# Performance work log

Hardware: AMD Instinct MI355X
Metric: run time of the kernel (lower is better)

Reference implementation:

```python
import jax, jax.numpy as jnp
import numpy as np

B, H, W, C = 8, 128, 128, 256
NH = 8
HD = C // NH
WS = 8           # window size
SS = 4           # shift size
N = WS * WS      # tokens per window
SCALE = HD ** -0.5
EPS = 1e-5


def _rel_pos_index():
    coords = np.stack(np.meshgrid(np.arange(WS), np.arange(WS), indexing='ij'))  # [2,WS,WS]
    cf = coords.reshape(2, -1)                                                   # [2,N]
    rel = (cf[:, :, None] - cf[:, None, :]).transpose(1, 2, 0)                   # [N,N,2]
    rel[..., 0] += WS - 1
    rel[..., 1] += WS - 1
    rel[..., 0] *= 2 * WS - 1
    return rel.sum(-1)  # [N,N] indices into (2*WS-1)^2 table

RPI = jnp.asarray(_rel_pos_index())


def _attn_mask():
    img = np.zeros((H, W))
    slices = (slice(0, -WS), slice(-WS, -SS), slice(-SS, None))
    cnt = 0
    for hs in slices:
        for ws_ in slices:
            img[hs, ws_] = cnt
            cnt += 1
    mw = img.reshape(H // WS, WS, W // WS, WS).transpose(0, 2, 1, 3).reshape(-1, N)  # [nW,N]
    am = mw[:, None, :] - mw[:, :, None]
    return jnp.asarray(np.where(am != 0, -100.0, 0.0).astype(np.float32))  # [nW,N,N]

ATTN_MASK = _attn_mask()


def _ln(x, g, b):
    m = jnp.mean(x, -1, keepdims=True)
    v = jnp.var(x, -1, keepdims=True)
    return (x - m) * jax.lax.rsqrt(v + EPS) * g + b


def setup_inputs() -> dict:
    key = jax.random.key(0)
    ks = jax.random.split(key, 8)
    s = 0.02
    return {
        'x': jax.random.normal(ks[0], (B, H * W, C), jnp.float32),
        'qkv_w': jax.random.normal(ks[1], (C, 3 * C), jnp.float32) * s,
        'qkv_b': jnp.zeros((3 * C,), jnp.float32),
        'proj_w': jax.random.normal(ks[2], (C, C), jnp.float32) * s,
        'proj_b': jnp.zeros((C,), jnp.float32),
        'rpb': jax.random.normal(ks[3], ((2 * WS - 1) ** 2, NH), jnp.float32) * s,
        'g1': jnp.ones((C,), jnp.float32), 'b1': jnp.zeros((C,), jnp.float32),
        'g2': jnp.ones((C,), jnp.float32), 'b2': jnp.zeros((C,), jnp.float32),
        'fc1_w': jax.random.normal(ks[4], (C, 4 * C), jnp.float32) * s,
        'fc1_b': jnp.zeros((4 * C,), jnp.float32),
        'fc2_w': jax.random.normal(ks[5], (4 * C, C), jnp.float32) * s,
        'fc2_b': jnp.zeros((C,), jnp.float32),
    }


def reference(x, qkv_w, qkv_b, proj_w, proj_b, rpb, g1, b1, g2, b2,
              fc1_w, fc1_b, fc2_w, fc2_b):
    nW = (H // WS) * (W // WS)
    shortcut = x
    h = _ln(x, g1, b1).reshape(B, H, W, C)
    # cyclic shift
    h = jnp.roll(h, (-SS, -SS), axis=(1, 2))
    # window partition -> (B*nW, N, C)
    win = h.reshape(B, H // WS, WS, W // WS, WS, C).transpose(0, 1, 3, 2, 4, 5).reshape(-1, N, C)
    qkv = (win @ qkv_w + qkv_b).reshape(-1, N, 3, NH, HD).transpose(2, 0, 3, 1, 4)  # [3,B_,NH,N,HD]
    q, k, v = qkv[0] * SCALE, qkv[1], qkv[2]
    attn = jnp.einsum('bhnd,bhmd->bhnm', q, k)                    # [B_,NH,N,N]
    bias = rpb[RPI].transpose(2, 0, 1)                             # [NH,N,N]
    attn = attn + bias[None]
    attn = attn.reshape(B, nW, NH, N, N) + ATTN_MASK[None, :, None]
    attn = jax.nn.softmax(attn.reshape(-1, NH, N, N), axis=-1)
    out = jnp.einsum('bhnm,bhmd->bhnd', attn, v).transpose(0, 2, 1, 3).reshape(-1, N, C)
    out = out @ proj_w + proj_b
    # window reverse + reverse shift
    out = out.reshape(B, H // WS, W // WS, WS, WS, C).transpose(0, 1, 3, 2, 4, 5).reshape(B, H, W, C)
    out = jnp.roll(out, (SS, SS), axis=(1, 2)).reshape(B, H * W, C)
    x = shortcut + out
    hm = _ln(x, g2, b2)
    hm = jax.nn.gelu(hm @ fc1_w + fc1_b, approximate=False) @ fc2_w + fc2_b
    return x + hm
```

## Files before the change

### kernel.cpp

```cpp
#include <hip/hip_runtime.h>
#include <math.h>


#define NWIN_TOTAL 2048
#define TOK_TOTAL  131072
#define SCALE_Q    0.17677669529663687f
#define LOG2E      1.4426950408889634f

typedef unsigned short u16;
typedef __attribute__((ext_vector_type(4))) unsigned short u16x4;
typedef __attribute__((ext_vector_type(8))) unsigned short u16x8;
typedef __attribute__((ext_vector_type(8))) short bf16x8;
typedef __attribute__((ext_vector_type(4))) float f32x4;

#define AS1 __attribute__((address_space(1)))
#define AS3 __attribute__((address_space(3)))
#define GLOAD_LDS16(g, l) \
  __builtin_amdgcn_global_load_lds((const AS1 unsigned int*)(g), (AS3 unsigned int*)(l), 16, 0, 0)

__device__ __forceinline__ float bf2f(u16 u) {
  union { unsigned int i; float f; } c; c.i = ((unsigned int)u) << 16; return c.f;
}
__device__ __forceinline__ u16 f2bf(float f) {
  union { float f; unsigned int i; } c; c.f = f;
  return (u16)((c.i + 0x7fff + ((c.i >> 16) & 1)) >> 16);
}
__device__ __forceinline__ int regid3(int h) { return h < 120 ? 0 : (h < 124 ? 1 : 2); }
__device__ __forceinline__ float gelu_f(float v) {
  float t = exp2f(v * fmaf(v * v, 0.10294423f, 2.3022082f));
  return v * t * __builtin_amdgcn_rcpf(t + 1.0f);
}

__device__ __forceinline__ int win_tok_to_t(int g, int n) {
  int b = g >> 8, wi = g & 255;
  int wr = wi >> 4, wc = wi & 15;
  int hs = wr * 8 + (n >> 3), ws2 = wc * 8 + (n & 7);
  int h = (hs + 4) & 127, w = (ws2 + 4) & 127;
  return (b << 14) + (h << 7) + w;
}

__global__ __launch_bounds__(256)
void wconv_kernel(const float* __restrict__ w, u16* __restrict__ wt, int K, int N)
{
  int i = blockIdx.x * 256 + threadIdx.x;
  if (i >= K * N) return;
  int k = i / N, n = i - k * N;
  wt[(size_t)n * K + k] = f2bf(w[i]);
}

__global__ __launch_bounds__(1024)
void qln_kernel(const float* __restrict__ x, const float* __restrict__ g1,
                const float* __restrict__ b1, const u16* __restrict__ qkvT,
                const float* __restrict__ qkv_b,
                u16* __restrict__ qb, u16* __restrict__ kb, u16* __restrict__ vb,
                int g0)
{
  __shared__ u16 Aln[16384];
  const int tid = threadIdx.x, wid = tid >> 6, lane = tid & 63;
  const int l15 = lane & 15, g = lane >> 4;
  const int bwi = blockIdx.x;
  const int gw = g0 + bwi;

  {
    const int row = tid >> 4;
    const int cq = (tid & 15) * 16;
    const int t = win_tok_to_t(gw, row);
    const float* src = x + (size_t)t * 256 + cq;
    float vals[16];
    float s = 0.f, q = 0.f;
#pragma unroll
    for (int i = 0; i < 4; ++i) {
      float4 v = ((const float4*)src)[i];
      vals[i*4] = v.x; vals[i*4+1] = v.y; vals[i*4+2] = v.z; vals[i*4+3] = v.w;
      s += v.x + v.y + v.z + v.w;
      q += v.x*v.x + v.y*v.y + v.z*v.z + v.w*v.w;
    }
    s += __shfl_xor(s, 1, 64); q += __shfl_xor(q, 1, 64);
    s += __shfl_xor(s, 2, 64); q += __shfl_xor(q, 2, 64);
    s += __shfl_xor(s, 4, 64); q += __shfl_xor(q, 4, 64);
    s += __shfl_xor(s, 8, 64); q += __shfl_xor(q, 8, 64);
    float mean = s * 0.00390625f;
    float rstd = rsqrtf(q * 0.00390625f - mean * mean + 1e-5f);
#pragma unroll
    for (int i = 0; i < 2; ++i) {
      const int col = cq + i * 8;
      u16x8 o;
#pragma unroll
      for (int j = 0; j < 8; ++j)
        o[j] = f2bf((vals[i*8+j] - mean) * rstd * g1[col+j] + b1[col+j]);
      const int gran = col >> 3;
      *(u16x8*)((char*)Aln + row * 512 + ((gran ^ (row & 7)) << 4)) = o;
    }
  }
  __syncthreads();

  f32x4 acc[4][3];
#pragma unroll
  for (int m = 0; m < 4; ++m)
#pragma unroll
    for (int n = 0; n < 3; ++n) acc[m][n] = (f32x4){0.f, 0.f, 0.f, 0.f};
  const int colb = wid * 48;
#pragma unroll
  for (int ks = 0; ks < 8; ++ks) {
    bf16x8 af[4], bw[3];
#pragma unroll
    for (int m = 0; m < 4; ++m) {
      const int tok = m * 16 + l15;
      const int gran = ks * 4 + g;
      af[m] = *(const bf16x8*)&Aln[tok * 256 + ((gran ^ (tok & 7)) << 3)];
    }
#pragma unroll
    for (int n = 0; n < 3; ++n)
      bw[n] = *(const bf16x8*)(qkvT + (size_t)(colb + n * 16 + l15) * 256 + ks * 32 + g * 8);
#pragma unroll
    for (int m = 0; m < 4; ++m)
#pragma unroll
      for (int n = 0; n < 3; ++n)
        acc[m][n] = __builtin_amdgcn_mfma_f32_16x16x32_bf16(af[m], bw[n], acc[m][n], 0, 0, 0);
  }

#pragma unroll
  for (int n = 0; n < 3; ++n) {
    const int col16 = colb + n * 16;
    const float bv = qkv_b[col16 + l15];
    const int s = col16 >> 8, head = (col16 >> 5) & 7, hd = col16 & 31;
    if (s == 2) {
      const size_t obase = ((size_t)bwi << 14) + ((size_t)head << 11) + (size_t)(hd + l15) * 64;
#pragma unroll
      for (int m = 0; m < 4; ++m) {
        const int tok0 = m * 16 + g * 4;
        u16x4 pk;
#pragma unroll
        for (int r = 0; r < 4; ++r) pk[r] = f2bf(acc[m][n][r] + bv);
        *(u16x4*)&vb[obase + tok0] = pk;
      }
    } else {
      u16* qdst = (s == 0) ? qb : kb;
      const float scl = (s == 0) ? SCALE_Q * LOG2E : 1.f;
      const size_t obase = ((size_t)bwi << 14) + ((size_t)head << 11) + hd + l15;
#pragma unroll
      for (int m = 0; m < 4; ++m)
#pragma unroll
        for (int r = 0; r < 4; ++r) {
          const int tok = m * 16 + g * 4 + r;
          qdst[obase + ((size_t)tok << 5)] = f2bf((acc[m][n][r] + bv) * scl);
        }
    }
  }
}

__global__ __launch_bounds__(512)
void awp_kernel(const u16* __restrict__ qb, const u16* __restrict__ kb,
                const u16* __restrict__ vt, const float* __restrict__ rpb,
                const u16* __restrict__ pjT, const float* __restrict__ pjb,
                const float* __restrict__ x, float* __restrict__ out, int g0)
{
  __shared__ union {
    u16 pl[8][2048];
    u16 aoL[16384];
    float rep[8192];
  } sb;
  __shared__ float rl[1800];
  const int tid = threadIdx.x, hh = tid >> 6, lane = tid & 63;
  const int l15 = lane & 15, g = lane >> 4;
  const int bw = blockIdx.x;

  for (int i = tid; i < 1800; i += 512) {
    unsigned int h2 = (unsigned)i / 225u;
    unsigned int rem = (unsigned)i - h2 * 225u;
    unsigned int aa = rem / 15u, bb = rem - aa * 15u;
    rl[i] = rpb[(aa * 15u + 14u - bb) * 8u + h2] * LOG2E;
  }
  __syncthreads();

  const size_t base = ((size_t)(bw * 8 + hh)) << 11;

  bf16x8 qf[4], kf[4];
#pragma unroll
  for (int f = 0; f < 4; ++f) {
    qf[f] = *(const bf16x8*)(qb + base + (size_t)(f * 16 + l15) * 32 + g * 8);
    kf[f] = *(const bf16x8*)(kb + base + (size_t)(f * 16 + l15) * 32 + g * 8);
  }
  f32x4 acc[4][4];
#pragma unroll
  for (int mf = 0; mf < 4; ++mf)
#pragma unroll
    for (int nf = 0; nf < 4; ++nf) acc[mf][nf] = (f32x4){0.f, 0.f, 0.f, 0.f};
#pragma unroll
  for (int mf = 0; mf < 4; ++mf)
#pragma unroll
    for (int nf = 0; nf < 4; ++nf)
      acc[mf][nf] = __builtin_amdgcn_mfma_f32_16x16x32_bf16(kf[mf], qf[nf], acc[mf][nf], 0, 0, 0);

  const int gwin = g0 + bw;
  const int wrw = (gwin >> 4) & 15, wcw = gwin & 15;
  const bool edge = (wrw == 15) || (wcw == 15);
  const int i2b = g >> 1;
  const int j2b = (g & 1) * 4;
#pragma unroll
  for (int nf = 0; nf < 4; ++nf) {
    const int n = nf * 16 + l15;
    const int i1 = n >> 3, j1 = n & 7;
    const int rid1 = edge ? regid3(wrw * 8 + i1) * 3 + regid3(wcw * 8 + j1) : 0;
#pragma unroll
    for (int mf = 0; mf < 4; ++mf) {
      const int i2 = mf * 2 + i2b;
      const int ib = hh * 225 + (i1 - i2 + 7) * 15 + (j2b - j1 + 7);
      const int r2a = edge ? regid3(wrw * 8 + i2) * 3 : 0;
#pragma unroll
      for (int r = 0; r < 4; ++r) {
        float b = rl[ib + r];
        if (edge) {
          int rid2 = r2a + regid3(wcw * 8 + j2b + r);
          if (rid2 != rid1) b -= 144.2695f;
        }
        acc[mf][nf][r] += b;
      }
    }
  }

  float inv[4];
#pragma unroll
  for (int nf = 0; nf < 4; ++nf) {
    float m0 = -1e30f;
#pragma unroll
    for (int mf = 0; mf < 4; ++mf)
#pragma unroll
      for (int r = 0; r < 4; ++r) m0 = fmaxf(m0, acc[mf][nf][r]);
    m0 = fmaxf(m0, __shfl_xor(m0, 16, 64));
    m0 = fmaxf(m0, __shfl_xor(m0, 32, 64));
    float s = 0.f;
#pragma unroll
    for (int mf = 0; mf < 4; ++mf)
#pragma unroll
      for (int r = 0; r < 4; ++r) {
        float p = exp2f(acc[mf][nf][r] - m0);
        acc[mf][nf][r] = p;
        s += p;
      }
    s += __shfl_xor(s, 16, 64);
    s += __shfl_xor(s, 32, 64);
    inv[nf] = 1.f / s;
  }

  bf16x8 vf[2][2];
#pragma unroll
  for (int df = 0; df < 2; ++df)
#pragma unroll
    for (int ks = 0; ks < 2; ++ks)
      vf[df][ks] = *(const bf16x8*)(vt + base + (size_t)(df * 16 + l15) * 64 + ks * 32 + g * 8);
  f32x4 accO[4][2];
#pragma unroll
  for (int nf = 0; nf < 4; ++nf)
#pragma unroll
    for (int df = 0; df < 2; ++df) accO[nf][df] = (f32x4){0.f, 0.f, 0.f, 0.f};
  char* plw = (char*)sb.pl[hh];
#pragma unroll
  for (int ks = 0; ks < 2; ++ks) {
#pragma unroll
    for (int nf = 0; nf < 4; ++nf) {
      const int n = nf * 16 + l15;
      const int swz = (n & 3) << 4;
#pragma unroll
      for (int mm = 0; mm < 2; ++mm) {
        const int mf = ks * 2 + mm;
        float p0 = acc[mf][nf][0] * inv[nf], p1 = acc[mf][nf][1] * inv[nf];
        float p2 = acc[mf][nf][2] * inv[nf], p3 = acc[mf][nf][3] * inv[nf];
        unsigned int pa, pb;
        asm("v_cvt_pk_bf16_f32 %0, %1, %2" : "=v"(pa) : "v"(p0), "v"(p1));
        asm("v_cvt_pk_bf16_f32 %0, %1, %2" : "=v"(pb) : "v"(p2), "v"(p3));
        uint2 w; w.x = pa; w.y = pb;
        *(uint2*)(plw + ((n * 64 + mm * 32 + g * 8) ^ swz)) = w;
      }
    }
#pragma unroll
    for (int nf = 0; nf < 4; ++nf) {
      const int n = nf * 16 + l15;
      const int swz = (n & 3) << 4;
      bf16x8 pf = *(const bf16x8*)(plw + ((n * 64 + g * 16) ^ swz));
#pragma unroll
      for (int df = 0; df < 2; ++df)
        accO[nf][df] = __builtin_amdgcn_mfma_f32_16x16x32_bf16(pf, vf[df][ks], accO[nf][df], 0, 0, 0);
    }
  }

  __syncthreads();
#pragma unroll
  for (int nf = 0; nf < 4; ++nf)
#pragma unroll
    for (int r = 0; r < 4; ++r) {
      const int tok = nf * 16 + g * 4 + r;
#pragma unroll
      for (int df = 0; df < 2; ++df) {
        const int ch = hh * 32 + df * 16 + l15;
        *(u16*)((char*)sb.aoL + tok * 512 + ((((ch >> 3) ^ (tok & 7))) << 4) + (ch & 7) * 2) =
            f2bf(accO[nf][df][r]);
      }
    }
  __syncthreads();

  float4 xv[2][4];
  {
    const int rowl = tid >> 4, coll = (tid & 15) * 16;
#pragma unroll
    for (int hp = 0; hp < 2; ++hp) {
      const int t = win_tok_to_t(g0 + bw, hp * 32 + rowl);
      const float* xs = x + (size_t)t * 256 + coll;
#pragma unroll
      for (int i = 0; i < 4; ++i) xv[hp][i] = ((const float4*)xs)[i];
    }
  }

  f32x4 pacc[4][2];
#pragma unroll
  for (int mf = 0; mf < 4; ++mf)
#pragma unroll
    for (int of = 0; of < 2; ++of) pacc[mf][of] = (f32x4){0.f, 0.f, 0.f, 0.f};
  const u16* pB = pjT + (size_t)(hh * 32) * 256;
#pragma unroll
  for (int ks = 0; ks < 8; ++ks) {
    bf16x8 af[4], bwf[2];
#pragma unroll
    for (int mf = 0; mf < 4; ++mf) {
      const int tok = mf * 16 + l15;
      af[mf] = *(const bf16x8*)((char*)sb.aoL + tok * 512 + (((ks * 4 + g) ^ (tok & 7)) << 4));
    }
#pragma unroll
    for (int of = 0; of < 2; ++of)
      bwf[of] = *(const bf16x8*)(pB + (size_t)(of * 16 + l15) * 256 + ks * 32 + g * 8);
#pragma unroll
    for (int mf = 0; mf < 4; ++mf)
#pragma unroll
      for (int of = 0; of < 2; ++of)
        pacc[mf][of] = __builtin_amdgcn_mfma_f32_16x16x32_bf16(af[mf], bwf[of], pacc[mf][of], 0, 0, 0);
  }

#pragma unroll
  for (int hp = 0; hp < 2; ++hp) {
    __syncthreads();
#pragma unroll
    for (int mm = 0; mm < 2; ++mm) {
      const int mf = hp * 2 + mm;
#pragma unroll
      for (int of = 0; of < 2; ++of) {
        const int oc = hh * 32 + of * 16 + l15;
        const float bv = pjb[oc];
#pragma unroll
        for (int r = 0; r < 4; ++r) {
          const int row = mm * 16 + g * 4 + r;
          *(float*)((char*)sb.rep + ((row * 1024 + oc * 4) ^ ((row & 3) << 4))) =
              pacc[mf][of][r] + bv;
        }
      }
    }
    __syncthreads();
    const int rowl = tid >> 4, coll = (tid & 15) * 16;
    const int tok = hp * 32 + rowl;
    const int t = win_tok_to_t(g0 + bw, tok);
    float* od = out + (size_t)t * 256 + coll;
#pragma unroll
    for (int i = 0; i < 4; ++i) {
      float4 rv = *(const float4*)((char*)sb.rep +
                    ((rowl * 1024 + (coll + i * 4) * 4) ^ ((rowl & 3) << 4)));
      ((float4*)od)[i] = make_float4(rv.x + xv[hp][i].x, rv.y + xv[hp][i].y,
                                     rv.z + xv[hp][i].z, rv.w + xv[hp][i].w);
    }
  }
}

__global__ __launch_bounds__(512)
void mlp_kernel(float* io, const u16* __restrict__ w1t, const u16* __restrict__ w2t,
                const float* __restrict__ fb1, const float* __restrict__ fb2,
                const float* __restrict__ g2, const float* __restrict__ bt2)
{
  __shared__ u16 Aln[16384];
  __shared__ u16 Hs[2][8192];
  const int tid = threadIdx.x, wid = tid >> 6, lane = tid & 63;
  const int l15 = lane & 15, g = lane >> 4;
  const int t0 = blockIdx.x * 64;

  {
    const int row = tid >> 3;
    const int cq = (tid & 7) * 32;
    const float* src = io + (size_t)(t0 + row) * 256 + cq;
    float vals[32];
    float s = 0.f, q = 0.f;
#pragma unroll
    for (int i = 0; i < 8; ++i) {
      float4 v = ((const float4*)src)[i];
      vals[i*4] = v.x; vals[i*4+1] = v.y; vals[i*4+2] = v.z; vals[i*4+3] = v.w;
      s += v.x + v.y + v.z + v.w;
      q += v.x*v.x + v.y*v.y + v.z*v.z + v.w*v.w;
    }
    s += __shfl_xor(s, 1, 64); q += __shfl_xor(q, 1, 64);
    s += __shfl_xor(s, 2, 64); q += __shfl_xor(q, 2, 64);
    s += __shfl_xor(s, 4, 64); q += __shfl_xor(q, 4, 64);
    float mean = s * 0.00390625f;
    float rstd = rsqrtf(q * 0.00390625f - mean * mean + 1e-5f);
#pragma unroll
    for (int i = 0; i < 4; ++i) {
      const int col = cq + i * 8;
      u16x8 o;
#pragma unroll
      for (int j = 0; j < 8; ++j)
        o[j] = f2bf((vals[i*8+j] - mean) * rstd * g2[col+j] + bt2[col+j]);
      const int gran = col >> 3;
      *(u16x8*)((char*)Aln + row * 512 + ((gran ^ (row & 7)) << 4)) = o;
    }
  }

  f32x4 acc2[4][2];
#pragma unroll
  for (int m = 0; m < 4; ++m)
#pragma unroll
    for (int n = 0; n < 2; ++n) acc2[m][n] = (f32x4){0.f, 0.f, 0.f, 0.f};
  f32x4 acc1[4];

#define MGEMM1(c)                                                                 \
  {                                                                               \
    _Pragma("unroll")                                                             \
    for (int tf = 0; tf < 4; ++tf) acc1[tf] = (f32x4){0.f, 0.f, 0.f, 0.f};        \
    const u16* w1base = w1t + (size_t)((c) * 128 + wid * 16) * 256;               \
    _Pragma("unroll")                                                             \
    for (int ks = 0; ks < 8; ++ks) {                                              \
      bf16x8 af = *(const bf16x8*)(w1base + (size_t)l15 * 256 + ks * 32 + g * 8); \
      bf16x8 bfr[4];                                                              \
      _Pragma("unroll")                                                           \
      for (int tf = 0; tf < 4; ++tf) {                                            \
        const int tok = tf * 16 + l15;                                            \
        const int gran = ks * 4 + g;                                              \
        bfr[tf] = *(const bf16x8*)&Aln[tok * 256 + ((gran ^ (tok & 7)) << 3)];    \
      }                                                                           \
      _Pragma("unroll")                                                           \
      for (int tf = 0; tf < 4; ++tf)                                              \
        acc1[tf] = __builtin_amdgcn_mfma_f32_16x16x32_bf16(af, bfr[tf], acc1[tf], 0, 0, 0); \
    }                                                                             \
  }

#define MPACK(c)                                                                  \
  {                                                                               \
    char* hdst = (char*)Hs[(c) & 1];                                              \
    const int hcl = wid * 16 + g * 4;                                             \
    const float b0 = fb1[(c) * 128 + hcl];                                        \
    const float b1 = fb1[(c) * 128 + hcl + 1];                                    \
    const float b2v = fb1[(c) * 128 + hcl + 2];                                   \
    const float b3 = fb1[(c) * 128 + hcl + 3];                                    \
    _Pragma("unroll")                                                             \
    for (int tf = 0; tf < 4; ++tf) {                                              \
      const int tok = tf * 16 + l15;                                              \
      float p0 = gelu_f(acc1[tf][0] + b0);                                        \
      float p1 = gelu_f(acc1[tf][1] + b1);                                        \
      float p2 = gelu_f(acc1[tf][2] + b2v);                                       \
      float p3 = gelu_f(acc1[tf][3] + b3);                                        \
      unsigned int pa, pb;                                                        \
      asm("v_cvt_pk_bf16_f32 %0, %1, %2" : "=v"(pa) : "v"(p0), "v"(p1));          \
      asm("v_cvt_pk_bf16_f32 %0, %1, %2" : "=v"(pb) : "v"(p2), "v"(p3));          \
      uint2 w; w.x = pa; w.y = pb;                                                \
      *(uint2*)(hdst + tok * 256 + (((hcl >> 3) ^ (tok & 7)) << 4) + ((hcl & 4) << 1)) = w; \
    }                                                                             \
  }

#define MGEMM2(c)                                                                 \
  {                                                                               \
    const u16* hsrc = Hs[(c) & 1];                                                \
    const u16* w2base = w2t + (size_t)(wid * 32) * 1024 + (c) * 128;              \
    _Pragma("unroll")                                                             \
    for (int hk = 0; hk < 4; ++hk) {                                              \
      bf16x8 ah[4], bw[2];                                                        \
      _Pragma("unroll")                                                           \
      for (int tf = 0; tf < 4; ++tf) {                                            \
        const int tok = tf * 16 + l15;                                            \
        const int gran = hk * 4 + g;                                              \
        ah[tf] = *(const bf16x8*)&hsrc[tok * 128 + ((gran ^ (tok & 7)) << 3)];    \
      }                                                                           \
      _Pragma("unroll")                                                           \
      for (int of = 0; of < 2; ++of)                                              \
        bw[of] = *(const bf16x8*)(w2base + (size_t)(of * 16 + l15) * 1024 + hk * 32 + g * 8); \
      _Pragma("unroll")                                                           \
      for (int tf = 0; tf < 4; ++tf)                                              \
        _Pragma("unroll")                                                         \
        for (int of = 0; of < 2; ++of)                                            \
          acc2[tf][of] = __builtin_amdgcn_mfma_f32_16x16x32_bf16(ah[tf], bw[of], acc2[tf][of], 0, 0, 0); \
    }                                                                             \
  }

  __syncthreads();
  MGEMM1(0);
  MPACK(0);
  __syncthreads();
#pragma unroll
  for (int c = 1; c < 8; ++c) {
    MGEMM2(c - 1);
    MGEMM1(c);
    MPACK(c);
    __syncthreads();
  }
  MGEMM2(7);
#undef MGEMM1
#undef MPACK
#undef MGEMM2

#pragma unroll
  for (int tf = 0; tf < 4; ++tf) {
#pragma unroll
    for (int of = 0; of < 2; ++of) {
      const int oc = wid * 32 + of * 16 + l15;
      const float bv = fb2[oc];
#pragma unroll
      for (int r = 0; r < 4; ++r) {
        const size_t off = (size_t)(t0 + tf * 16 + g * 4 + r) * 256 + oc;
        io[off] = acc2[tf][of][r] + bv + io[off];
      }
    }
  }
}

extern "C" void kernel_launch(void* const* d_in, const int* in_sizes, int n_in,
                              void* d_out, int out_size, void* d_ws, size_t ws_size,
                              hipStream_t stream)
{
  const float* x      = (const float*)d_in[0];
  const float* qkv_w  = (const float*)d_in[1];
  const float* qkv_b  = (const float*)d_in[2];
  const float* proj_w = (const float*)d_in[3];
  const float* proj_b = (const float*)d_in[4];
  const float* rpb    = (const float*)d_in[5];
  const float* g1     = (const float*)d_in[6];
  const float* b1     = (const float*)d_in[7];
  const float* g2     = (const float*)d_in[8];
  const float* b2     = (const float*)d_in[9];
  const float* fc1_w  = (const float*)d_in[10];
  const float* fc1_b  = (const float*)d_in[11];
  const float* fc2_w  = (const float*)d_in[12];
  const float* fc2_b  = (const float*)d_in[13];
  float* out = (float*)d_out;
  char* ws = (char*)d_ws;

  u16* qkvT  = (u16*)ws;
  u16* projT = qkvT + 196608;
  u16* fc1T  = projT + 65536;
  u16* fc2T  = fc1T + 262144;
  char* pb = (char*)(fc2T + 262144);
  size_t used = 1572864ULL;
  size_t R = ws_size > used ? ws_size - used : 0;

  wconv_kernel<<<(196608 + 255) / 256, 256, 0, stream>>>(qkv_w, qkvT, 256, 768);
  wconv_kernel<<<(65536  + 255) / 256, 256, 0, stream>>>(proj_w, projT, 256, 256);
  wconv_kernel<<<(262144 + 255) / 256, 256, 0, stream>>>(fc1_w, fc1T, 256, 1024);
  wconv_kernel<<<(262144 + 255) / 256, 256, 0, stream>>>(fc2_w, fc2T, 1024, 256);

  int Gc = 2048;
  while (Gc > 2 && (size_t)Gc * 98304ULL > R) Gc >>= 1;

  u16* qb = (u16*)pb;
  u16* kb = qb + (size_t)Gc * 16384;
  u16* vb = kb + (size_t)Gc * 16384;

  for (int g0 = 0; g0 < NWIN_TOTAL; g0 += Gc) {
    qln_kernel<<<Gc, 1024, 0, stream>>>(x, g1, b1, qkvT, qkv_b, qb, kb, vb, g0);
    awp_kernel<<<Gc, 512, 0, stream>>>(qb, kb, vb, rpb, projT, proj_b, x, out, g0);
  }

  mlp_kernel<<<TOK_TOTAL / 64, 512, 0, stream>>>(out, fc1T, fc2T, fc1_b, fc2_b, g2, b2);
}
```

Measured before the change: 641.4 us.

## Fuse LN+QKV and window attention+proj into one kernel with LDS staging

Merges the LN/QKV projection kernel and the attention+projection kernel into a single 1024-thread kernel per window. Q, K and V now stay in swizzled LDS instead of going through a global workspace, and the chunked launch loop is removed. Attention work is split across 16 waves (two token halves per head), and the output projection is split into 16 column slices. This removes a global write and read of QKV plus one launch per chunk. In exchange it uses more LDS per block, which may lower occupancy.

```diff
diff --git a/kernel.cpp b/kernel.cpp
--- a/kernel.cpp
+++ b/kernel.cpp
@@ -12,11 +12,6 @@
 typedef __attribute__((ext_vector_type(8))) unsigned short u16x8;
 typedef __attribute__((ext_vector_type(8))) short bf16x8;
 typedef __attribute__((ext_vector_type(4))) float f32x4;
-
-#define AS1 __attribute__((address_space(1)))
-#define AS3 __attribute__((address_space(3)))
-#define GLOAD_LDS16(g, l) \
-  __builtin_amdgcn_global_load_lds((const AS1 unsigned int*)(g), (AS3 unsigned int*)(l), 16, 0, 0)
 
 __device__ __forceinline__ float bf2f(u16 u) {
   union { unsigned int i; float f; } c; c.i = ((unsigned int)u) << 16; return c.f;
@@ -49,17 +44,33 @@
 }
 
 __global__ __launch_bounds__(1024)
-void qln_kernel(const float* __restrict__ x, const float* __restrict__ g1,
-                const float* __restrict__ b1, const u16* __restrict__ qkvT,
-                const float* __restrict__ qkv_b,
-                u16* __restrict__ qb, u16* __restrict__ kb, u16* __restrict__ vb,
-                int g0)
+void fawp_kernel(const float* __restrict__ x, const float* __restrict__ g1,
+                 const float* __restrict__ b1, const u16* __restrict__ qkvT,
+                 const float* __restrict__ qkv_b, const float* __restrict__ rpb,
+                 const u16* __restrict__ pjT, const float* __restrict__ pjb,
+                 float* __restrict__ out)
 {
-  __shared__ u16 Aln[16384];
+  __shared__ u16 QL[8][2048];
+  __shared__ u16 KL[8][2048];
+  __shared__ u16 VL[8][2048];
+  __shared__ union {
+    u16 Aln[16384];
+    u16 pl[16][1024];
+    u16 aoL[16384];
+    float rep[8192];
+  } sb;
+  __shared__ float rl[1800];
+
   const int tid = threadIdx.x, wid = tid >> 6, lane = tid & 63;
   const int l15 = lane & 15, g = lane >> 4;
-  const int bwi = blockIdx.x;
-  const int gw = g0 + bwi;
+  const int gw = blockIdx.x;
+
+  for (int i = tid; i < 1800; i += 1024) {
+    unsigned int h2 = (unsigned)i / 225u;
+    unsigned int rem = (unsigned)i - h2 * 225u;
+    unsigned int aa = rem / 15u, bb = rem - aa * 15u;
+    rl[i] = rpb[(aa * 15u + 14u - bb) * 8u + h2] * LOG2E;
+  }
 
   {
     const int row = tid >> 4;
@@ -89,279 +100,262 @@
       for (int j = 0; j < 8; ++j)
         o[j] = f2bf((vals[i*8+j] - mean) * rstd * g1[col+j] + b1[col+j]);
       const int gran = col >> 3;
-      *(u16x8*)((char*)Aln + row * 512 + ((gran ^ (row & 7)) << 4)) = o;
+      *(u16x8*)((char*)sb.Aln + row * 512 + ((gran ^ (row & 7)) << 4)) = o;
     }
   }
   __syncthreads();
 
-  f32x4 acc[4][3];
-#pragma unroll
-  for (int m = 0; m < 4; ++m)
-#pragma unroll
-    for (int n = 0; n < 3; ++n) acc[m][n] = (f32x4){0.f, 0.f, 0.f, 0.f};
-  const int colb = wid * 48;
-#pragma unroll
-  for (int ks = 0; ks < 8; ++ks) {
-    bf16x8 af[4], bw[3];
-#pragma unroll
-    for (int m = 0; m < 4; ++m) {
-      const int tok = m * 16 + l15;
-      const int gran = ks * 4 + g;
-      af[m] = *(const bf16x8*)&Aln[tok * 256 + ((gran ^ (tok & 7)) << 3)];
-    }
-#pragma unroll
-    for (int n = 0; n < 3; ++n)
-      bw[n] = *(const bf16x8*)(qkvT + (size_t)(colb + n * 16 + l15) * 256 + ks * 32 + g * 8);
+  {
+    f32x4 acc[4][3];
 #pragma unroll
     for (int m = 0; m < 4; ++m)
 #pragma unroll
+      for (int n = 0; n < 3; ++n) acc[m][n] = (f32x4){0.f, 0.f, 0.f, 0.f};
+    const int colb = wid * 48;
+#pragma unroll
+    for (int ks = 0; ks < 8; ++ks) {
+      bf16x8 af[4], bw[3];
+#pragma unroll
+      for (int m = 0; m < 4; ++m) {
+        const int tok = m * 16 + l15;
+        const int gran = ks * 4 + g;
+        af[m] = *(const bf16x8*)&sb.Aln[tok * 256 + ((gran ^ (tok & 7)) << 3)];
+      }
+#pragma unroll
       for (int n = 0; n < 3; ++n)
-        acc[m][n] = __builtin_amdgcn_mfma_f32_16x16x32_bf16(af[m], bw[n], acc[m][n], 0, 0, 0);
-  }
-
-#pragma unroll
-  for (int n = 0; n < 3; ++n) {
-    const int col16 = colb + n * 16;
-    const float bv = qkv_b[col16 + l15];
-    const int s = col16 >> 8, head = (col16 >> 5) & 7, hd = col16 & 31;
-    if (s == 2) {
-      const size_t obase = ((size_t)bwi << 14) + ((size_t)head << 11) + (size_t)(hd + l15) * 64;
-#pragma unroll
-      for (int m = 0; m < 4; ++m) {
-        const int tok0 = m * 16 + g * 4;
-        u16x4 pk;
-#pragma unroll
-        for (int r = 0; r < 4; ++r) pk[r] = f2bf(acc[m][n][r] + bv);
-        *(u16x4*)&vb[obase + tok0] = pk;
-      }
-    } else {
-      u16* qdst = (s == 0) ? qb : kb;
-      const float scl = (s == 0) ? SCALE_Q * LOG2E : 1.f;
-      const size_t obase = ((size_t)bwi << 14) + ((size_t)head << 11) + hd + l15;
+        bw[n] = *(const bf16x8*)(qkvT + (size_t)(colb + n * 16 + l15) * 256 + ks * 32 + g * 8);
 #pragma unroll
       for (int m = 0; m < 4; ++m)
 #pragma unroll
+        for (int n = 0; n < 3; ++n)
+          acc[m][n] = __builtin_amdgcn_mfma_f32_16x16x32_bf16(af[m], bw[n], acc[m][n], 0, 0, 0);
+    }
+
+#pragma unroll
+    for (int n = 0; n < 3; ++n) {
+      const int col16 = colb + n * 16;
+      const float bv = qkv_b[col16 + l15];
+      const int s = col16 >> 8, head = (col16 >> 5) & 7, hd = col16 & 31;
+      if (s == 2) {
+        const int row = hd + l15;
+        char* vdst = (char*)VL[head] + row * 128;
+        const int sw = (row & 7) << 4;
+#pragma unroll
+        for (int m = 0; m < 4; ++m) {
+          const int tok0 = m * 16 + g * 4;
+          u16x4 pk;
+#pragma unroll
+          for (int r = 0; r < 4; ++r) pk[r] = f2bf(acc[m][n][r] + bv);
+          *(u16x4*)(vdst + ((tok0 * 2) ^ sw)) = pk;
+        }
+      } else {
+        char* dstL = (char*)((s == 0) ? QL[head] : KL[head]);
+        const float scl = (s == 0) ? SCALE_Q * LOG2E : 1.f;
+        const int cb2 = (hd + l15) * 2;
+#pragma unroll
+        for (int m = 0; m < 4; ++m)
+#pragma unroll
+          for (int r = 0; r < 4; ++r) {
+            const int tok = m * 16 + g * 4 + r;
+            *(u16*)(dstL + tok * 64 + (cb2 ^ (((tok >> 1) & 3) << 4))) =
+                f2bf((acc[m][n][r] + bv) * scl);
+          }
+      }
+    }
+  }
+  __syncthreads();
+
+  const int hh = wid & 7, half = wid >> 3;
+  f32x4 accO[2][2];
+  {
+    bf16x8 qf[2], kf[4];
+#pragma unroll
+    for (int nfl = 0; nfl < 2; ++nfl) {
+      const int n = half * 32 + nfl * 16 + l15;
+      qf[nfl] = *(const bf16x8*)((char*)QL[hh] + n * 64 + ((g * 16) ^ (((n >> 1) & 3) << 4)));
+    }
+#pragma unroll
+    for (int f = 0; f < 4; ++f) {
+      const int m = f * 16 + l15;
+      kf[f] = *(const bf16x8*)((char*)KL[hh] + m * 64 + ((g * 16) ^ (((m >> 1) & 3) << 4)));
+    }
+    f32x4 acc[4][2];
+#pragma unroll
+    for (int mf = 0; mf < 4; ++mf)
+#pragma unroll
+      for (int nfl = 0; nfl < 2; ++nfl) acc[mf][nfl] = (f32x4){0.f, 0.f, 0.f, 0.f};
+#pragma unroll
+    for (int mf = 0; mf < 4; ++mf)
+#pragma unroll
+      for (int nfl = 0; nfl < 2; ++nfl)
+        acc[mf][nfl] = __builtin_amdgcn_mfma_f32_16x16x32_bf16(kf[mf], qf[nfl], acc[mf][nfl], 0, 0, 0);
+
+    const int wrw = (gw >> 4) & 15, wcw = gw & 15;
+    const bool edge = (wrw == 15) || (wcw == 15);
+    const int i2b = g >> 1;
+    const int j2b = (g & 1) * 4;
+#pragma unroll
+    for (int nfl = 0; nfl < 2; ++nfl) {
+      const int n = half * 32 + nfl * 16 + l15;
+      const int i1 = n >> 3, j1 = n & 7;
+      const int rid1 = edge ? regid3(wrw * 8 + i1) * 3 + regid3(wcw * 8 + j1) : 0;
+#pragma unroll
+      for (int mf = 0; mf < 4; ++mf) {
+        const int i2 = mf * 2 + i2b;
+        const int ib = hh * 225 + (i1 - i2 + 7) * 15 + (j2b - j1 + 7);
+        const int r2a = edge ? regid3(wrw * 8 + i2) * 3 : 0;
+#pragma unroll
         for (int r = 0; r < 4; ++r) {
-          const int tok = m * 16 + g * 4 + r;
-          qdst[obase + ((size_t)tok << 5)] = f2bf((acc[m][n][r] + bv) * scl);
+          float b = rl[ib + r];
+          if (edge) {
+            int rid2 = r2a + regid3(wcw * 8 + j2b + r);
+            if (rid2 != rid1) b -= 144.2695f;
+          }
+          acc[mf][nfl][r] += b;
         }
-    }
-  }
-}
-
-__global__ __launch_bounds__(512)
-void awp_kernel(const u16* __restrict__ qb, const u16* __restrict__ kb,
-                const u16* __restrict__ vt, const float* __restrict__ rpb,
-                const u16* __restrict__ pjT, const float* __restrict__ pjb,
-                const float* __restrict__ x, float* __restrict__ out, int g0)
-{
-  __shared__ union {
-    u16 pl[8][2048];
-    u16 aoL[16384];
-    float rep[8192];
-  } sb;
-  __shared__ float rl[1800];
-  const int tid = threadIdx.x, hh = tid >> 6, lane = tid & 63;
-  const int l15 = lane & 15, g = lane >> 4;
-  const int bw = blockIdx.x;
-
-  for (int i = tid; i < 1800; i += 512) {
-    unsigned int h2 = (unsigned)i / 225u;
-    unsigned int rem = (unsigned)i - h2 * 225u;
-    unsigned int aa = rem / 15u, bb = rem - aa * 15u;
-    rl[i] = rpb[(aa * 15u + 14u - bb) * 8u + h2] * LOG2E;
-  }
+      }
+    }
+
+    float inv[2];
+#pragma unroll
+    for (int nfl = 0; nfl < 2; ++nfl) {
+      float m0 = -1e30f;
+#pragma unroll
+      for (int mf = 0; mf < 4; ++mf)
+#pragma unroll
+        for (int r = 0; r < 4; ++r) m0 = fmaxf(m0, acc[mf][nfl][r]);
+      m0 = fmaxf(m0, __shfl_xor(m0, 16, 64));
+      m0 = fmaxf(m0, __shfl_xor(m0, 32, 64));
+      float s = 0.f;
+#pragma unroll
+      for (int mf = 0; mf < 4; ++mf)
+#pragma unroll
+        for (int r = 0; r < 4; ++r) {
+          float p = exp2f(acc[mf][nfl][r] - m0);
+          acc[mf][nfl][r] = p;
+          s += p;
+        }
+      s += __shfl_xor(s, 16, 64);
+      s += __shfl_xor(s, 32, 64);
+      inv[nfl] = 1.f / s;
+    }
+
+    bf16x8 vf[2][2];
+#pragma unroll
+    for (int df = 0; df < 2; ++df)
+#pragma unroll
+      for (int ks = 0; ks < 2; ++ks) {
+        const int row = df * 16 + l15;
+        vf[df][ks] = *(const bf16x8*)((char*)VL[hh] + row * 128 +
+                       ((ks * 64 + g * 16) ^ ((row & 7) << 4)));
+      }
+#pragma unroll
+    for (int nfl = 0; nfl < 2; ++nfl)
+#pragma unroll
+      for (int df = 0; df < 2; ++df) accO[nfl][df] = (f32x4){0.f, 0.f, 0.f, 0.f};
+    char* plw = (char*)sb.pl[wid];
+#pragma unroll
+    for (int ks = 0; ks < 2; ++ks) {
+#pragma unroll
+      for (int nfl = 0; nfl < 2; ++nfl) {
+        const int nloc = nfl * 16 + l15;
+        const int swz = (nloc & 3) << 4;
+#pragma unroll
+        for (int mm = 0; mm < 2; ++mm) {
+          const int mf = ks * 2 + mm;
+          float p0 = acc[mf][nfl][0] * inv[nfl], p1 = acc[mf][nfl][1] * inv[nfl];
+          float p2 = acc[mf][nfl][2] * inv[nfl], p3 = acc[mf][nfl][3] * inv[nfl];
+          unsigned int pa, pb;
+          asm("v_cvt_pk_bf16_f32 %0, %1, %2" : "=v"(pa) : "v"(p0), "v"(p1));
+          asm("v_cvt_pk_bf16_f32 %0, %1, %2" : "=v"(pb) : "v"(p2), "v"(p3));
+          uint2 w; w.x = pa; w.y = pb;
+          *(uint2*)(plw + ((nloc * 64 + mm * 32 + g * 8) ^ swz)) = w;
+        }
+      }
+#pragma unroll
+      for (int nfl = 0; nfl < 2; ++nfl) {
+        const int nloc = nfl * 16 + l15;
+        const int swz = (nloc & 3) << 4;
+        bf16x8 pf = *(const bf16x8*)(plw + ((nloc * 64 + g * 16) ^ swz));
+#pragma unroll
+        for (int df = 0; df < 2; ++df)
+          accO[nfl][df] = __builtin_amdgcn_mfma_f32_16x16x32_bf16(pf, vf[df][ks], accO[nfl][df], 0, 0, 0);
+      }
+    }
+  }
+
   __syncthreads();
-
-  const size_t base = ((size_t)(bw * 8 + hh)) << 11;
-
-  bf16x8 qf[4], kf[4];
-#pragma unroll
-  for (int f = 0; f < 4; ++f) {
-    qf[f] = *(const bf16x8*)(qb + base + (size_t)(f * 16 + l15) * 32 + g * 8);
-    kf[f] = *(const bf16x8*)(kb + base + (size_t)(f * 16 + l15) * 32 + g * 8);
-  }
-  f32x4 acc[4][4];
-#pragma unroll
-  for (int mf = 0; mf < 4; ++mf)
-#pragma unroll
-    for (int nf = 0; nf < 4; ++nf) acc[mf][nf] = (f32x4){0.f, 0.f, 0.f, 0.f};
-#pragma unroll
-  for (int mf = 0; mf < 4; ++mf)
-#pragma unroll
-    for (int nf = 0; nf < 4; ++nf)
-      acc[mf][nf] = __builtin_amdgcn_mfma_f32_16x16x32_bf16(kf[mf], qf[nf], acc[mf][nf], 0, 0, 0);
-
-  const int gwin = g0 + bw;
-  const int wrw = (gwin >> 4) & 15, wcw = gwin & 15;
-  const bool edge = (wrw == 15) || (wcw == 15);
-  const int i2b = g >> 1;
-  const int j2b = (g & 1) * 4;
-#pragma unroll
-  for (int nf = 0; nf < 4; ++nf) {
-    const int n = nf * 16 + l15;
-    const int i1 = n >> 3, j1 = n & 7;
-    const int rid1 = edge ? regid3(wrw * 8 + i1) * 3 + regid3(wcw * 8 + j1) : 0;
-#pragma unroll
-    for (int mf = 0; mf < 4; ++mf) {
-      const int i2 = mf * 2 + i2b;
-      const int ib = hh * 225 + (i1 - i2 + 7) * 15 + (j2b - j1 + 7);
-      const int r2a = edge ? regid3(wrw * 8 + i2) * 3 : 0;
-#pragma unroll
-      for (int r = 0; r < 4; ++r) {
-        float b = rl[ib + r];
-        if (edge) {
-          int rid2 = r2a + regid3(wcw * 8 + j2b + r);
-          if (rid2 != rid1) b -= 144.2695f;
-        }
-        acc[mf][nf][r] += b;
-      }
-    }
-  }
-
-  float inv[4];
-#pragma unroll
-  for (int nf = 0; nf < 4; ++nf) {
-    float m0 = -1e30f;
-#pragma unroll
-    for (int mf = 0; mf < 4; ++mf)
-#pragma unroll
-      for (int r = 0; r < 4; ++r) m0 = fmaxf(m0, acc[mf][nf][r]);
-    m0 = fmaxf(m0, __shfl_xor(m0, 16, 64));
-    m0 = fmaxf(m0, __shfl_xor(m0, 32, 64));
-    float s = 0.f;
-#pragma unroll
-    for (int mf = 0; mf < 4; ++mf)
-#pragma unroll
-      for (int r = 0; r < 4; ++r) {
-        float p = exp2f(acc[mf][nf][r] - m0);
-        acc[mf][nf][r] = p;
-        s += p;
-      }
-    s += __shfl_xor(s, 16, 64);
-    s += __shfl_xor(s, 32, 64);
-    inv[nf] = 1.f / s;
-  }
-
-  bf16x8 vf[2][2];
-#pragma unroll
-  for (int df = 0; df < 2; ++df)
-#pragma unroll
-    for (int ks = 0; ks < 2; ++ks)
-      vf[df][ks] = *(const bf16x8*)(vt + base + (size_t)(df * 16 + l15) * 64 + ks * 32 + g * 8);
-  f32x4 accO[4][2];
-#pragma unroll
-  for (int nf = 0; nf < 4; ++nf)
-#pragma unroll
-    for (int df = 0; df < 2; ++df) accO[nf][df] = (f32x4){0.f, 0.f, 0.f, 0.f};
-  char* plw = (char*)sb.pl[hh];
-#pragma unroll
-  for (int ks = 0; ks < 2; ++ks) {
-#pragma unroll
-    for (int nf = 0; nf < 4; ++nf) {
-      const int n = nf * 16 + l15;
-      const int swz = (n & 3) << 4;
-#pragma unroll
-      for (int mm = 0; mm < 2; ++mm) {
-        const int mf = ks * 2 + mm;
-        float p0 = acc[mf][nf][0] * inv[nf], p1 = acc[mf][nf][1] * inv[nf];
-        float p2 = acc[mf][nf][2] * inv[nf], p3 = acc[mf][nf][3] * inv[nf];
-        unsigned int pa, pb;
-        asm("v_cvt_pk_bf16_f32 %0, %1, %2" : "=v"(pa) : "v"(p0), "v"(p1));
-        asm("v_cvt_pk_bf16_f32 %0, %1, %2" : "=v"(pb) : "v"(p2), "v"(p3));
-        uint2 w; w.x = pa; w.y = pb;
-        *(uint2*)(plw + ((n * 64 + mm * 32 + g * 8) ^ swz)) = w;
-      }
-    }
-#pragma unroll
-    for (int nf = 0; nf < 4; ++nf) {
-      const int n = nf * 16 + l15;
-      const int swz = (n & 3) << 4;
-      bf16x8 pf = *(const bf16x8*)(plw + ((n * 64 + g * 16) ^ swz));
-#pragma unroll
-      for (int df = 0; df < 2; ++df)
-        accO[nf][df] = __builtin_amdgcn_mfma_f32_16x16x32_bf16(pf, vf[df][ks], accO[nf][df], 0, 0, 0);
-    }
-  }
-
-  __syncthreads();
-#pragma unroll
-  for (int nf = 0; nf < 4; ++nf)
+#pragma unroll
+  for (int nfl = 0; nfl < 2; ++nfl)
 #pragma unroll
     for (int r = 0; r < 4; ++r) {
-      const int tok = nf * 16 + g * 4 + r;
+      const int tok = half * 32 + nfl * 16 + g * 4 + r;
 #pragma unroll
       for (int df = 0; df < 2; ++df) {
         const int ch = hh * 32 + df * 16 + l15;
         *(u16*)((char*)sb.aoL + tok * 512 + ((((ch >> 3) ^ (tok & 7))) << 4) + (ch & 7) * 2) =
-            f2bf(accO[nf][df][r]);
+            f2bf(accO[nfl][df][r]);
       }
     }
   __syncthreads();
 
-  float4 xv[2][4];
+  float4 xv[2][2];
   {
-    const int rowl = tid >> 4, coll = (tid & 15) * 16;
+    const int prow = tid >> 5, pcolb = (tid & 31) * 8;
 #pragma unroll
     for (int hp = 0; hp < 2; ++hp) {
-      const int t = win_tok_to_t(g0 + bw, hp * 32 + rowl);
-      const float* xs = x + (size_t)t * 256 + coll;
-#pragma unroll
-      for (int i = 0; i < 4; ++i) xv[hp][i] = ((const float4*)xs)[i];
-    }
-  }
-
-  f32x4 pacc[4][2];
-#pragma unroll
-  for (int mf = 0; mf < 4; ++mf)
-#pragma unroll
-    for (int of = 0; of < 2; ++of) pacc[mf][of] = (f32x4){0.f, 0.f, 0.f, 0.f};
-  const u16* pB = pjT + (size_t)(hh * 32) * 256;
-#pragma unroll
-  for (int ks = 0; ks < 8; ++ks) {
-    bf16x8 af[4], bwf[2];
-#pragma unroll
-    for (int mf = 0; mf < 4; ++mf) {
-      const int tok = mf * 16 + l15;
-      af[mf] = *(const bf16x8*)((char*)sb.aoL + tok * 512 + (((ks * 4 + g) ^ (tok & 7)) << 4));
-    }
-#pragma unroll
-    for (int of = 0; of < 2; ++of)
-      bwf[of] = *(const bf16x8*)(pB + (size_t)(of * 16 + l15) * 256 + ks * 32 + g * 8);
-#pragma unroll
-    for (int mf = 0; mf < 4; ++mf)
-#pragma unroll
-      for (int of = 0; of < 2; ++of)
-        pacc[mf][of] = __builtin_amdgcn_mfma_f32_16x16x32_bf16(af[mf], bwf[of], pacc[mf][of], 0, 0, 0);
+      const int t = win_tok_to_t(gw, hp * 32 + prow);
+      const float* xs = x + (size_t)t * 256 + pcolb;
+      xv[hp][0] = ((const float4*)xs)[0];
+      xv[hp][1] = ((const float4*)xs)[1];
+    }
+  }
+
+  f32x4 pacc[4];
+#pragma unroll
+  for (int mf = 0; mf < 4; ++mf) pacc[mf] = (f32x4){0.f, 0.f, 0.f, 0.f};
+  {
+    const u16* pB = pjT + (size_t)(wid * 16 + l15) * 256;
+#pragma unroll
+    for (int ks = 0; ks < 8; ++ks) {
+      bf16x8 af[4];
+#pragma unroll
+      for (int mf = 0; mf < 4; ++mf) {
+        const int tok = mf * 16 + l15;
+        af[mf] = *(const bf16x8*)((char*)sb.aoL + tok * 512 + (((ks * 4 + g) ^ (tok & 7)) << 4));
+      }
+      bf16x8 bwf = *(const bf16x8*)(pB + ks * 32 + g * 8);
+#pragma unroll
+      for (int mf = 0; mf < 4; ++mf)
+        pacc[mf] = __builtin_amdgcn_mfma_f32_16x16x32_bf16(af[mf], bwf, pacc[mf], 0, 0, 0);
+    }
   }
 
 #pragma unroll
   for (int hp = 0; hp < 2; ++hp) {
     __syncthreads();
-#pragma unroll
-    for (int mm = 0; mm < 2; ++mm) {
-      const int mf = hp * 2 + mm;
-#pragma unroll
-      for (int of = 0; of < 2; ++of) {
-        const int oc = hh * 32 + of * 16 + l15;
-        const float bv = pjb[oc];
+    {
+      const int oc = wid * 16 + l15;
+      const float bv = pjb[oc];
+#pragma unroll
+      for (int mm = 0; mm < 2; ++mm) {
+        const int mf = hp * 2 + mm;
 #pragma unroll
         for (int r = 0; r < 4; ++r) {
           const int row = mm * 16 + g * 4 + r;
           *(float*)((char*)sb.rep + ((row * 1024 + oc * 4) ^ ((row & 3) << 4))) =
-              pacc[mf][of][r] + bv;
+              pacc[mf][r] + bv;
         }
       }
     }
     __syncthreads();
-    const int rowl = tid >> 4, coll = (tid & 15) * 16;
-    const int tok = hp * 32 + rowl;
-    const int t = win_tok_to_t(g0 + bw, tok);
-    float* od = out + (size_t)t * 256 + coll;
-#pragma unroll
-    for (int i = 0; i < 4; ++i) {
+    const int row = tid >> 5, colb = (tid & 31) * 8;
+    const int t = win_tok_to_t(gw, hp * 32 + row);
+    float* od = out + (size_t)t * 256 + colb;
+#pragma unroll
+    for (int i = 0; i < 2; ++i) {
       float4 rv = *(const float4*)((char*)sb.rep +
-                    ((rowl * 1024 + (coll + i * 4) * 4) ^ ((rowl & 3) << 4)));
+                    ((row * 1024 + (colb + i * 4) * 4) ^ ((row & 3) << 4)));
       ((float4*)od)[i] = make_float4(rv.x + xv[hp][i].x, rv.y + xv[hp][i].y,
                                      rv.z + xv[hp][i].z, rv.w + xv[hp][i].w);
     }
@@ -540,26 +534,14 @@
   u16* projT = qkvT + 196608;
   u16* fc1T  = projT + 65536;
   u16* fc2T  = fc1T + 262144;
-  char* pb = (char*)(fc2T + 262144);
-  size_t used = 1572864ULL;
-  size_t R = ws_size > used ? ws_size - used : 0;
 
   wconv_kernel<<<(196608 + 255) / 256, 256, 0, stream>>>(qkv_w, qkvT, 256, 768);
   wconv_kernel<<<(65536  + 255) / 256, 256, 0, stream>>>(proj_w, projT, 256, 256);
   wconv_kernel<<<(262144 + 255) / 256, 256, 0, stream>>>(fc1_w, fc1T, 256, 1024);
   wconv_kernel<<<(262144 + 255) / 256, 256, 0, stream>>>(fc2_w, fc2T, 1024, 256);
 
-  int Gc = 2048;
-  while (Gc > 2 && (size_t)Gc * 98304ULL > R) Gc >>= 1;
-
-  u16* qb = (u16*)pb;
-  u16* kb = qb + (size_t)Gc * 16384;
-  u16* vb = kb + (size_t)Gc * 16384;
-
-  for (int g0 = 0; g0 < NWIN_TOTAL; g0 += Gc) {
-    qln_kernel<<<Gc, 1024, 0, stream>>>(x, g1, b1, qkvT, qkv_b, qb, kb, vb, g0);
-    awp_kernel<<<Gc, 512, 0, stream>>>(qb, kb, vb, rpb, projT, proj_b, x, out, g0);
-  }
+  fawp_kernel<<<NWIN_TOTAL, 1024, 0, stream>>>(x, g1, b1, qkvT, qkv_b, rpb,
+                                               projT, proj_b, out);
 
   mlp_kernel<<<TOK_TOTAL / 64, 512, 0, stream>>>(out, fc1T, fc2T, fc1_b, fc2_b, g2, b2);
 }
```

After: 572.8 us, median of 2. 10.7% less time.
